# Performance work log

Hardware: AMD Instinct MI355X
Metric: run time of the kernel (lower is better)

The kernel has to match this reference:

```python
import jax, jax.numpy as jnp
from jax import lax
import numpy as np

PAD = 0
V, DW, H, T, B = 30000, 512, 512, 50, 128


def _xavier(key, shape):
    fan_in, fan_out = shape[1], shape[0]
    lim = float(np.sqrt(6.0 / (fan_in + fan_out)))
    return jax.random.uniform(key, shape, jnp.float32, -lim, lim)


def setup_inputs() -> dict:
    key = jax.random.key(0)
    ks = jax.random.split(key, 8)
    return {
        "user": jax.random.randint(ks[0], (B,), 0, 10000),
        "item": jax.random.randint(ks[1], (B,), 0, 10000),
        "review_input": jax.random.randint(ks[2], (T, B), 0, V),
        "review_target": jax.random.randint(ks[3], (T, B), 0, V),
        "word_emb": jax.random.normal(ks[4], (V, DW), jnp.float32) * 0.02,
        "W_ih": _xavier(ks[5], (3 * H, DW)),
        "W_hh": _xavier(ks[6], (3 * H, H)),
        "b_ih": jnp.zeros((3 * H,), jnp.float32),
        "b_hh": jnp.zeros((3 * H,), jnp.float32),
        "W_out": _xavier(ks[7], (V, H)),
        "b_out": jnp.zeros((V,), jnp.float32),
    }


def reference(user, item, review_input, review_target,
              word_emb, W_ih, W_hh, b_ih, b_hh, W_out, b_out):
    n_batch = user.shape[0]
    # embed all timesteps at once: [T, B, DW]
    x = word_emb[review_input]
    # precompute input-to-gate projections: [T, B, 3H]
    xg = jnp.einsum('tbd,gd->tbg', x, W_ih) + b_ih
    h0 = jnp.zeros((n_batch, H), x.dtype)

    def step(h, xg_t):
        hg = h @ W_hh.T + b_hh                      # [B, 3H]
        xr, xz, xn = jnp.split(xg_t, 3, axis=-1)    # PyTorch order: r, z, n
        hr, hz, hn = jnp.split(hg, 3, axis=-1)
        r = jax.nn.sigmoid(xr + hr)
        z = jax.nn.sigmoid(xz + hz)
        n = jnp.tanh(xn + r * hn)
        h_new = (1.0 - z) * n + z * h
        return h_new, h_new

    _, outs = lax.scan(step, h0, xg)                # [T, B, H]
    logits = outs.reshape(-1, H) @ W_out.T + b_out  # [T*B, V]
    tgt = review_target.reshape(-1)
    logp = jax.nn.log_softmax(logits, axis=-1)
    nll = -jnp.take_along_axis(logp, tgt[:, None], axis=1)[:, 0]
    mask = tgt != PAD
    out_loss = jnp.where(mask, nll, 0.0)            # F.cross_entropy reduction='none', ignore_index=PAD
    denom = jnp.maximum(jnp.sum(mask), 1).astype(out_loss.dtype)
    obj = jnp.sum(out_loss) / denom                 # mean over non-ignored tokens
    return out_loss, obj
```

## Files before the change

### kernel.cpp

```cpp
#include <hip/hip_runtime.h>

typedef short short8 __attribute__((ext_vector_type(8)));
typedef float f32x4 __attribute__((ext_vector_type(4)));
typedef float f4 __attribute__((ext_vector_type(4)));
typedef unsigned short ushort_t;

#define VOCAB 30000
#define DW 512
#define KDIM 512
#define HDIM 512
#define G3 1536
#define TT 50
#define BB 128
#define M_ROWS 6400
#define NPAD 30208
#define NT2 472

__device__ __forceinline__ float b2f(ushort_t u){ return __uint_as_float(((unsigned)u)<<16); }
__device__ __forceinline__ ushort_t f2b(float f){
    unsigned u = __float_as_uint(f);
    unsigned r = (u + 0x7fffu + ((u>>16)&1u)) >> 16;
    return (ushort_t)r;
}
__device__ __forceinline__ float sigf(float x){
    float e = __expf(-x);
    return __builtin_amdgcn_rcpf(1.0f + e);
}
__device__ __forceinline__ float tanh_(float x){
    return 2.0f*sigf(2.0f*x) - 1.0f;
}
__device__ __forceinline__ void gload16(const ushort_t* g, char* l){
    __builtin_amdgcn_global_load_lds((const __attribute__((address_space(1))) void*)g,
                                     (__attribute__((address_space(3))) void*)l, 16, 0, 0);
}

__global__ void k_cvt4(const f4* __restrict__ s, ushort_t* __restrict__ d, int n4){
    int i = blockIdx.x*blockDim.x + threadIdx.x;
    if (i < n4){
        f4 v = s[i];
        unsigned lo = (unsigned)f2b(v[0]) | ((unsigned)f2b(v[1]) << 16);
        unsigned hi = (unsigned)f2b(v[2]) | ((unsigned)f2b(v[3]) << 16);
        *(uint2*)(d + (size_t)i*4) = make_uint2(lo, hi);
    }
}
__global__ void k_zero_u(ushort_t* __restrict__ d, int n){
    int i = blockIdx.x*blockDim.x + threadIdx.x;
    if (i < n) d[i] = 0;
}
__global__ void k_gather(const float* __restrict__ emb, const int* __restrict__ idx,
                         ushort_t* __restrict__ x){
    int row = blockIdx.x;
    int v = idx[row];
    const float2* src = (const float2*)(emb + (size_t)v*DW);
    unsigned* dst = (unsigned*)(x + (size_t)row*DW);
    for (int d = threadIdx.x; d < DW/2; d += blockDim.x){
        float2 w = src[d];
        dst[d] = (unsigned)f2b(w.x) | ((unsigned)f2b(w.y) << 16);
    }
}
__global__ void k_biasg(const float* __restrict__ bi, const float* __restrict__ bh,
                        float* __restrict__ bg, float* __restrict__ hf,
                        ushort_t* __restrict__ hb){
    int i = blockIdx.x*blockDim.x + threadIdx.x;
    if (i < G3) bg[i] = bi[i] + (i < 2*HDIM ? bh[i] : 0.0f);
    if (i < BB*HDIM){ hf[i] = 0.0f; hb[i] = 0; }
}

template<int MODE, int NBLK>
__global__ __launch_bounds__(256, 3) void k_gemm5(const ushort_t* __restrict__ A,
        const ushort_t* __restrict__ Bw, const float* __restrict__ bias,
        ushort_t* __restrict__ Cout, float* __restrict__ psum){
    __shared__ ushort_t As[128*32];
    __shared__ ushort_t Bs[128*32];
    const int nwg = NBLK * 50;
    const int q = nwg >> 3;
    int wgid = (blockIdx.x & 7)*q + (blockIdx.x >> 3);
    int band = wgid / (10*NBLK);
    int rr   = wgid % (10*NBLK);
    int nb = rr / 10;
    int mb = band*10 + (rr % 10);
    int n0 = nb*128, m0 = mb*128;

    int lane = threadIdx.x & 63, wv = threadIdx.x >> 6;
    int lo = lane & 15, hi = lane >> 4;
    int wr = wv >> 1, wc = wv & 1;
    f32x4 acc[4][4] = {};
    int xsl = ((lane & 3) ^ ((lane >> 3) & 3)) * 8;
    const ushort_t* gA = A  + (size_t)(m0 + wv*32 + (lane>>2))*KDIM + xsl;
    const ushort_t* gB = Bw + (size_t)(n0 + wv*32 + (lane>>2))*KDIM + xsl;
    char* lA = (char*)As + wv*2048;
    char* lB = (char*)Bs + wv*2048;
    int rchunk = (hi ^ ((lo >> 1) & 3)) * 8;
    for (int kt = 0; kt < 16; ++kt){
        __syncthreads();
        int k0 = kt*32;
        gload16(gA + k0,           lA);
        gload16(gA + 16*KDIM + k0, lA + 1024);
        gload16(gB + k0,           lB);
        gload16(gB + 16*KDIM + k0, lB + 1024);
        __syncthreads();
        short8 av[4], bv[4];
        #pragma unroll
        for (int mi = 0; mi < 4; ++mi)
            av[mi] = *(const short8*)&As[(wr*64 + mi*16 + lo)*32 + rchunk];
        #pragma unroll
        for (int ni = 0; ni < 4; ++ni)
            bv[ni] = *(const short8*)&Bs[(wc*64 + ni*16 + lo)*32 + rchunk];
        #pragma unroll
        for (int mi = 0; mi < 4; ++mi)
            #pragma unroll
            for (int ni = 0; ni < 4; ++ni)
                acc[mi][ni] = __builtin_amdgcn_mfma_f32_16x16x32_bf16(av[mi], bv[ni], acc[mi][ni], 0, 0, 0);
    }

    if (MODE == 0){
        #pragma unroll
        for (int ni = 0; ni < 4; ++ni){
            int n = n0 + wc*64 + ni*16 + lo;
            float bb = bias[n];
            #pragma unroll
            for (int mi = 0; mi < 4; ++mi){
                #pragma unroll
                for (int j = 0; j < 4; ++j){
                    int m = m0 + wr*64 + mi*16 + hi*4 + j;
                    Cout[(size_t)m*G3 + n] = f2b(acc[mi][ni][j] + bb);
                }
            }
        }
    } else {
        const int NT = NBLK*2;
        float bov[4];
        bool valid[4];
        #pragma unroll
        for (int ni = 0; ni < 4; ++ni){
            int col = n0 + wc*64 + ni*16 + lo;
            valid[ni] = (col < VOCAB);
            bov[ni] = valid[ni] ? bias[col] : 0.0f;
        }
        int tile = nb*2 + wc;
        #pragma unroll
        for (int mi = 0; mi < 4; ++mi){
            #pragma unroll
            for (int j = 0; j < 4; ++j){
                float s = 0.0f;
                #pragma unroll
                for (int ni = 0; ni < 4; ++ni)
                    s += valid[ni] ? __expf(acc[mi][ni][j] + bov[ni]) : 0.0f;
                for (int d = 1; d < 16; d <<= 1) s += __shfl_xor(s, d, 64);
                if (lo == 0){
                    int m = m0 + wr*64 + mi*16 + hi*4 + j;
                    psum[(size_t)m*NT + tile] = s;
                }
            }
        }
    }
}

__global__ __launch_bounds__(256) void k_step(const ushort_t* __restrict__ hprev_b,
        const float* __restrict__ hprev_f, const ushort_t* __restrict__ Whh,
        const ushort_t* __restrict__ xg, const float* __restrict__ bh,
        float* __restrict__ hnext_f, ushort_t* __restrict__ hnext_b,
        ushort_t* __restrict__ outs, int t){
    __shared__ float gl[3][4][16][17];
    int tid = threadIdx.x;
    int lane = tid & 63, wv = tid >> 6;
    int lo = lane & 15, hi = lane >> 4;
    int c16 = blockIdx.x * 16;
    int b0  = blockIdx.y * 16;
    f32x4 acc[3] = {};
    const ushort_t* Arow = hprev_b + (size_t)(b0 + lo)*HDIM + wv*128;
    const ushort_t* Bbase = Whh + (size_t)(c16 + lo)*HDIM + wv*128;
    #pragma unroll
    for (int kk = 0; kk < 4; ++kk){
        int k0 = kk*32 + hi*8;
        short8 a = *(const short8*)(Arow + k0);
        #pragma unroll
        for (int g = 0; g < 3; ++g){
            short8 b = *(const short8*)(Bbase + (size_t)g*HDIM*HDIM + k0);
            acc[g] = __builtin_amdgcn_mfma_f32_16x16x32_bf16(a, b, acc[g], 0, 0, 0);
        }
    }
    #pragma unroll
    for (int g = 0; g < 3; ++g)
        #pragma unroll
        for (int j = 0; j < 4; ++j)
            gl[g][wv][hi*4 + j][lo] = acc[g][j];
    __syncthreads();
    int b = tid >> 4, c = tid & 15;
    int bt = b0 + b, cc = c16 + c;
    float hr = gl[0][0][b][c] + gl[0][1][b][c] + gl[0][2][b][c] + gl[0][3][b][c];
    float hz = gl[1][0][b][c] + gl[1][1][b][c] + gl[1][2][b][c] + gl[1][3][b][c];
    float hn = gl[2][0][b][c] + gl[2][1][b][c] + gl[2][2][b][c] + gl[2][3][b][c];
    const ushort_t* xgt = xg + (size_t)t*BB*G3 + (size_t)bt*G3;
    float xr = b2f(xgt[cc]);
    float xz = b2f(xgt[HDIM + cc]);
    float xn = b2f(xgt[2*HDIM + cc]);
    float r  = sigf(hr + xr);
    float z  = sigf(hz + xz);
    float n  = tanh_(xn + r*(hn + bh[2*HDIM + cc]));
    float hold = hprev_f[(size_t)bt*HDIM + cc];
    float hnew = (1.0f - z)*n + z*hold;
    hnext_f[(size_t)bt*HDIM + cc] = hnew;
    ushort_t hv = f2b(hnew);
    hnext_b[(size_t)bt*HDIM + cc] = hv;
    outs[((size_t)t*BB + bt)*HDIM + cc] = hv;
}

__global__ __launch_bounds__(256) void k_loss(const ushort_t* __restrict__ outs,
        const ushort_t* __restrict__ Wo, const float* __restrict__ bo,
        const float* __restrict__ psum, const int* __restrict__ tgt,
        float* __restrict__ out){
    int lane = threadIdx.x & 63, wv = threadIdx.x >> 6;
    int row = blockIdx.x*4 + wv;
    int tg = tgt[row];
    const float* ps = psum + (size_t)row*NT2;
    float S = 0.0f;
    for (int t = lane; t < NT2; t += 64) S += ps[t];
    for (int d = 1; d < 64; d <<= 1) S += __shfl_xor(S, d, 64);
    float lse = __logf(S);
    const ushort_t* a = outs + (size_t)row*HDIM + lane*8;
    const ushort_t* w = Wo + (size_t)tg*DW + lane*8;
    float s = 0.0f;
    #pragma unroll
    for (int j = 0; j < 8; ++j) s += b2f(a[j]) * b2f(w[j]);
    for (int d = 1; d < 64; d <<= 1) s += __shfl_xor(s, d, 64);
    if (lane == 0){
        float logit = s + bo[tg];
        out[row] = (tg != 0) ? (lse - logit) : 0.0f;
    }
}

__global__ __launch_bounds__(1024) void k_obj(const float* __restrict__ loss,
        const int* __restrict__ tgt, float* __restrict__ out){
    __shared__ float ss[1024];
    __shared__ int   sc[1024];
    float s = 0.0f; int c = 0;
    for (int i = threadIdx.x; i < M_ROWS; i += 1024){
        s += loss[i];
        c += (tgt[i] != 0) ? 1 : 0;
    }
    ss[threadIdx.x] = s; sc[threadIdx.x] = c;
    __syncthreads();
    for (int d = 512; d > 0; d >>= 1){
        if (threadIdx.x < (unsigned)d){ ss[threadIdx.x] += ss[threadIdx.x+d]; sc[threadIdx.x] += sc[threadIdx.x+d]; }
        __syncthreads();
    }
    if (threadIdx.x == 0) out[M_ROWS] = ss[0] / (float)(sc[0] > 0 ? sc[0] : 1);
}

extern "C" void kernel_launch(void* const* d_in, const int* in_sizes, int n_in,
                              void* d_out, int out_size, void* d_ws, size_t ws_size,
                              hipStream_t stream) {
    const int*   review_input  = (const int*)d_in[2];
    const int*   review_target = (const int*)d_in[3];
    const float* word_emb = (const float*)d_in[4];
    const float* W_ih = (const float*)d_in[5];
    const float* W_hh = (const float*)d_in[6];
    const float* b_ih = (const float*)d_in[7];
    const float* b_hh = (const float*)d_in[8];
    const float* W_out = (const float*)d_in[9];
    const float* b_out = (const float*)d_in[10];
    float* out = (float*)d_out;
    (void)n_in; (void)in_sizes; (void)out_size; (void)ws_size;

    char* ws = (char*)d_ws;
    size_t off = 0;
    auto alloc = [&](size_t bytes)->char*{
        char* p = ws + off;
        off = (off + bytes + 255) & ~(size_t)255;
        return p;
    };
    ushort_t* Wout_b = (ushort_t*)alloc((size_t)NPAD*DW*2);
    ushort_t* Wih_b  = (ushort_t*)alloc((size_t)G3*DW*2);
    ushort_t* Whh_b  = (ushort_t*)alloc((size_t)G3*HDIM*2);
    ushort_t* outs_b = (ushort_t*)alloc((size_t)M_ROWS*HDIM*2);
    float*    biasg  = (float*)alloc((size_t)G3*4);
    float*    h_f    = (float*)alloc((size_t)2*BB*HDIM*4);
    ushort_t* h_b    = (ushort_t*)alloc((size_t)2*BB*HDIM*2);
    ushort_t* xb     = (ushort_t*)alloc((size_t)M_ROWS*DW*2);
    ushort_t* xg     = (ushort_t*)alloc((size_t)M_ROWS*G3*2);
    float*    psum   = (float*)xb;

    k_cvt4<<<(G3*DW/4+255)/256, 256, 0, stream>>>((const f4*)W_ih, Wih_b, G3*DW/4);
    k_cvt4<<<(G3*HDIM/4+255)/256, 256, 0, stream>>>((const f4*)W_hh, Whh_b, G3*HDIM/4);
    k_cvt4<<<(VOCAB*DW/4+255)/256, 256, 0, stream>>>((const f4*)W_out, Wout_b, VOCAB*DW/4);
    k_zero_u<<<((NPAD-VOCAB)*DW+255)/256, 256, 0, stream>>>(Wout_b + (size_t)VOCAB*DW, (NPAD-VOCAB)*DW);
    k_gather<<<M_ROWS, 256, 0, stream>>>(word_emb, review_input, xb);
    k_biasg<<<(BB*HDIM+255)/256, 256, 0, stream>>>(b_ih, b_hh, biasg, h_f, h_b);

    k_gemm5<0, 12><<<600, 256, 0, stream>>>(xb, Wih_b, biasg, xg, nullptr);

    for (int t = 0; t < TT; ++t){
        int cur = t & 1, nxt = cur ^ 1;
        k_step<<<dim3(HDIM/16, BB/16), 256, 0, stream>>>(h_b + (size_t)cur*BB*HDIM,
                                       h_f + (size_t)cur*BB*HDIM,
                                       Whh_b, xg, b_hh,
                                       h_f + (size_t)nxt*BB*HDIM,
                                       h_b + (size_t)nxt*BB*HDIM,
                                       outs_b, t);
    }

    k_gemm5<1, 236><<<11800, 256, 0, stream>>>(outs_b, Wout_b, b_out, nullptr, psum);
    k_loss<<<M_ROWS/4, 256, 0, stream>>>(outs_b, Wout_b, b_out, psum, review_target, out);
    k_obj<<<1, 1024, 0, stream>>>(out, review_target, out);
}
```

Measured before the change: 513.7 us.

## Overlap output-projection GEMM with GRU recurrence steps in fused per-step kernel

Merges the GRU step kernel and the vocabulary GEMM with partial softmax sums into one kernel launched once per timestep. The first 256 blocks advance the recurrence for step t, while 236 more blocks compute logits and exp-sums for the 128 rows produced at step t-1. This spreads the large output GEMM across the otherwise underused serial recurrence and fills idle CUs. The GEMM tile now uses a 64-wide K slice with XOR swizzle. The cost is larger LDS per block, which can lower occupancy for the step blocks, and mixed work within one launch.

Result: slower. 754.5 us (+46.9%).

```diff
diff --git a/kernel.cpp b/kernel.cpp
--- a/kernel.cpp
+++ b/kernel.cpp
@@ -14,6 +14,7 @@
 #define BB 128
 #define M_ROWS 6400
 #define NPAD 30208
+#define NTILE 236
 #define NT2 472
 
 __device__ __forceinline__ float b2f(ushort_t u){ return __uint_as_float(((unsigned)u)<<16); }
@@ -66,10 +67,10 @@
     if (i < BB*HDIM){ hf[i] = 0.0f; hb[i] = 0; }
 }
 
-template<int MODE, int NBLK>
-__global__ __launch_bounds__(256, 3) void k_gemm5(const ushort_t* __restrict__ A,
+template<int NBLK>
+__global__ __launch_bounds__(256, 3) void k_gemmA(const ushort_t* __restrict__ A,
         const ushort_t* __restrict__ Bw, const float* __restrict__ bias,
-        ushort_t* __restrict__ Cout, float* __restrict__ psum){
+        ushort_t* __restrict__ Cout){
     __shared__ ushort_t As[128*32];
     __shared__ ushort_t Bs[128*32];
     const int nwg = NBLK * 50;
@@ -112,98 +113,148 @@
             for (int ni = 0; ni < 4; ++ni)
                 acc[mi][ni] = __builtin_amdgcn_mfma_f32_16x16x32_bf16(av[mi], bv[ni], acc[mi][ni], 0, 0, 0);
     }
-
-    if (MODE == 0){
-        #pragma unroll
-        for (int ni = 0; ni < 4; ++ni){
-            int n = n0 + wc*64 + ni*16 + lo;
-            float bb = bias[n];
-            #pragma unroll
-            for (int mi = 0; mi < 4; ++mi){
-                #pragma unroll
-                for (int j = 0; j < 4; ++j){
-                    int m = m0 + wr*64 + mi*16 + hi*4 + j;
-                    Cout[(size_t)m*G3 + n] = f2b(acc[mi][ni][j] + bb);
-                }
+    #pragma unroll
+    for (int ni = 0; ni < 4; ++ni){
+        int n = n0 + wc*64 + ni*16 + lo;
+        float bb = bias[n];
+        #pragma unroll
+        for (int mi = 0; mi < 4; ++mi){
+            #pragma unroll
+            for (int j = 0; j < 4; ++j){
+                int m = m0 + wr*64 + mi*16 + hi*4 + j;
+                Cout[(size_t)m*G3 + n] = f2b(acc[mi][ni][j] + bb);
             }
         }
-    } else {
-        const int NT = NBLK*2;
-        float bov[4];
-        bool valid[4];
-        #pragma unroll
-        for (int ni = 0; ni < 4; ++ni){
-            int col = n0 + wc*64 + ni*16 + lo;
-            valid[ni] = (col < VOCAB);
-            bov[ni] = valid[ni] ? bias[col] : 0.0f;
-        }
-        int tile = nb*2 + wc;
-        #pragma unroll
-        for (int mi = 0; mi < 4; ++mi){
-            #pragma unroll
-            for (int j = 0; j < 4; ++j){
-                float s = 0.0f;
-                #pragma unroll
-                for (int ni = 0; ni < 4; ++ni)
-                    s += valid[ni] ? __expf(acc[mi][ni][j] + bov[ni]) : 0.0f;
-                for (int d = 1; d < 16; d <<= 1) s += __shfl_xor(s, d, 64);
-                if (lo == 0){
-                    int m = m0 + wr*64 + mi*16 + hi*4 + j;
-                    psum[(size_t)m*NT + tile] = s;
-                }
-            }
-        }
-    }
-}
-
-__global__ __launch_bounds__(256) void k_step(const ushort_t* __restrict__ hprev_b,
-        const float* __restrict__ hprev_f, const ushort_t* __restrict__ Whh,
-        const ushort_t* __restrict__ xg, const float* __restrict__ bh,
-        float* __restrict__ hnext_f, ushort_t* __restrict__ hnext_b,
-        ushort_t* __restrict__ outs, int t){
+    }
+}
+
+__global__ __launch_bounds__(256) void k_fused(
+        const ushort_t* __restrict__ hprev_b, const float* __restrict__ hprev_f,
+        const ushort_t* __restrict__ Whh, const ushort_t* __restrict__ xg,
+        const float* __restrict__ bh, float* __restrict__ hnext_f,
+        ushort_t* __restrict__ hnext_b, ushort_t* __restrict__ outs,
+        const ushort_t* __restrict__ Wo, const float* __restrict__ bo,
+        float* __restrict__ psum, int t){
+    __shared__ ushort_t As[128*64];
+    __shared__ ushort_t Bs[128*64];
     __shared__ float gl[3][4][16][17];
     int tid = threadIdx.x;
     int lane = tid & 63, wv = tid >> 6;
     int lo = lane & 15, hi = lane >> 4;
-    int c16 = blockIdx.x * 16;
-    int b0  = blockIdx.y * 16;
-    f32x4 acc[3] = {};
-    const ushort_t* Arow = hprev_b + (size_t)(b0 + lo)*HDIM + wv*128;
-    const ushort_t* Bbase = Whh + (size_t)(c16 + lo)*HDIM + wv*128;
+
+    if (blockIdx.x < 256){
+        if (t >= TT) return;
+        int c16 = (blockIdx.x & 31) * 16;
+        int b0  = (blockIdx.x >> 5) * 16;
+        f32x4 acc[3] = {};
+        const ushort_t* Arow = hprev_b + (size_t)(b0 + lo)*HDIM + wv*128;
+        const ushort_t* Bbase = Whh + (size_t)(c16 + lo)*HDIM + wv*128;
+        #pragma unroll
+        for (int kk = 0; kk < 4; ++kk){
+            int k0 = kk*32 + hi*8;
+            short8 a = *(const short8*)(Arow + k0);
+            #pragma unroll
+            for (int g = 0; g < 3; ++g){
+                short8 b = *(const short8*)(Bbase + (size_t)g*HDIM*HDIM + k0);
+                acc[g] = __builtin_amdgcn_mfma_f32_16x16x32_bf16(a, b, acc[g], 0, 0, 0);
+            }
+        }
+        #pragma unroll
+        for (int g = 0; g < 3; ++g)
+            #pragma unroll
+            for (int j = 0; j < 4; ++j)
+                gl[g][wv][hi*4 + j][lo] = acc[g][j];
+        __syncthreads();
+        int b = tid >> 4, c = tid & 15;
+        int bt = b0 + b, cc = c16 + c;
+        float hr = gl[0][0][b][c] + gl[0][1][b][c] + gl[0][2][b][c] + gl[0][3][b][c];
+        float hz = gl[1][0][b][c] + gl[1][1][b][c] + gl[1][2][b][c] + gl[1][3][b][c];
+        float hn = gl[2][0][b][c] + gl[2][1][b][c] + gl[2][2][b][c] + gl[2][3][b][c];
+        const ushort_t* xgt = xg + (size_t)t*BB*G3 + (size_t)bt*G3;
+        float xr = b2f(xgt[cc]);
+        float xz = b2f(xgt[HDIM + cc]);
+        float xn = b2f(xgt[2*HDIM + cc]);
+        float r  = sigf(hr + xr);
+        float z  = sigf(hz + xz);
+        float n  = tanh_(xn + r*(hn + bh[2*HDIM + cc]));
+        float hold = hprev_f[(size_t)bt*HDIM + cc];
+        float hnew = (1.0f - z)*n + z*hold;
+        hnext_f[(size_t)bt*HDIM + cc] = hnew;
+        ushort_t hv = f2b(hnew);
+        hnext_b[(size_t)bt*HDIM + cc] = hv;
+        outs[((size_t)t*BB + bt)*HDIM + cc] = hv;
+        return;
+    }
+
+    if (t == 0) return;
+    int nb = blockIdx.x - 256;
+    int tm = t - 1;
+    int m0 = tm * 128;
+    int n0 = nb * 128;
+    int wr = wv >> 1, wc = wv & 1;
+    f32x4 acc[4][4] = {};
+    int srow = lane >> 3;
+    int xslot = (lane & 7) ^ srow;
+    const ushort_t* gA = outs + (size_t)(m0 + wv*32 + srow)*KDIM + xslot*8;
+    const ushort_t* gB = Wo   + (size_t)(n0 + wv*32 + srow)*KDIM + xslot*8;
+    char* lA = (char*)As + (size_t)(wv*32)*128;
+    char* lB = (char*)Bs + (size_t)(wv*32)*128;
+    for (int kt = 0; kt < 8; ++kt){
+        __syncthreads();
+        int k0 = kt*64;
+        #pragma unroll
+        for (int cc4 = 0; cc4 < 4; ++cc4){
+            gload16(gA + (size_t)cc4*8*KDIM + k0, lA + cc4*8*128);
+            gload16(gB + (size_t)cc4*8*KDIM + k0, lB + cc4*8*128);
+        }
+        __syncthreads();
+        short8 av[4][2], bv[4][2];
+        #pragma unroll
+        for (int mi = 0; mi < 4; ++mi){
+            int rrow = wr*64 + mi*16 + lo;
+            #pragma unroll
+            for (int ks = 0; ks < 2; ++ks)
+                av[mi][ks] = *(const short8*)&As[rrow*64 + (((ks*4+hi) ^ (lo&7)))*8];
+        }
+        #pragma unroll
+        for (int ni = 0; ni < 4; ++ni){
+            int rrow = wc*64 + ni*16 + lo;
+            #pragma unroll
+            for (int ks = 0; ks < 2; ++ks)
+                bv[ni][ks] = *(const short8*)&Bs[rrow*64 + (((ks*4+hi) ^ (lo&7)))*8];
+        }
+        #pragma unroll
+        for (int mi = 0; mi < 4; ++mi)
+            #pragma unroll
+            for (int ni = 0; ni < 4; ++ni){
+                acc[mi][ni] = __builtin_amdgcn_mfma_f32_16x16x32_bf16(av[mi][0], bv[ni][0], acc[mi][ni], 0, 0, 0);
+                acc[mi][ni] = __builtin_amdgcn_mfma_f32_16x16x32_bf16(av[mi][1], bv[ni][1], acc[mi][ni], 0, 0, 0);
+            }
+    }
+    float bov[4];
+    bool valid[4];
     #pragma unroll
-    for (int kk = 0; kk < 4; ++kk){
-        int k0 = kk*32 + hi*8;
-        short8 a = *(const short8*)(Arow + k0);
-        #pragma unroll
-        for (int g = 0; g < 3; ++g){
-            short8 b = *(const short8*)(Bbase + (size_t)g*HDIM*HDIM + k0);
-            acc[g] = __builtin_amdgcn_mfma_f32_16x16x32_bf16(a, b, acc[g], 0, 0, 0);
-        }
-    }
+    for (int ni = 0; ni < 4; ++ni){
+        int col = n0 + wc*64 + ni*16 + lo;
+        valid[ni] = (col < VOCAB);
+        bov[ni] = valid[ni] ? bo[col] : 0.0f;
+    }
+    int tile = nb*2 + wc;
     #pragma unroll
-    for (int g = 0; g < 3; ++g)
-        #pragma unroll
-        for (int j = 0; j < 4; ++j)
-            gl[g][wv][hi*4 + j][lo] = acc[g][j];
-    __syncthreads();
-    int b = tid >> 4, c = tid & 15;
-    int bt = b0 + b, cc = c16 + c;
-    float hr = gl[0][0][b][c] + gl[0][1][b][c] + gl[0][2][b][c] + gl[0][3][b][c];
-    float hz = gl[1][0][b][c] + gl[1][1][b][c] + gl[1][2][b][c] + gl[1][3][b][c];
-    float hn = gl[2][0][b][c] + gl[2][1][b][c] + gl[2][2][b][c] + gl[2][3][b][c];
-    const ushort_t* xgt = xg + (size_t)t*BB*G3 + (size_t)bt*G3;
-    float xr = b2f(xgt[cc]);
-    float xz = b2f(xgt[HDIM + cc]);
-    float xn = b2f(xgt[2*HDIM + cc]);
-    float r  = sigf(hr + xr);
-    float z  = sigf(hz + xz);
-    float n  = tanh_(xn + r*(hn + bh[2*HDIM + cc]));
-    float hold = hprev_f[(size_t)bt*HDIM + cc];
-    float hnew = (1.0f - z)*n + z*hold;
-    hnext_f[(size_t)bt*HDIM + cc] = hnew;
-    ushort_t hv = f2b(hnew);
-    hnext_b[(size_t)bt*HDIM + cc] = hv;
-    outs[((size_t)t*BB + bt)*HDIM + cc] = hv;
+    for (int mi = 0; mi < 4; ++mi){
+        #pragma unroll
+        for (int j = 0; j < 4; ++j){
+            float s = 0.0f;
+            #pragma unroll
+            for (int ni = 0; ni < 4; ++ni)
+                s += valid[ni] ? __expf(acc[mi][ni][j] + bov[ni]) : 0.0f;
+            for (int d = 1; d < 16; d <<= 1) s += __shfl_xor(s, d, 64);
+            if (lo == 0){
+                int m = m0 + wr*64 + mi*16 + hi*4 + j;
+                psum[(size_t)m*NT2 + tile] = s;
+            }
+        }
+    }
 }
 
 __global__ __launch_bounds__(256) void k_loss(const ushort_t* __restrict__ outs,
@@ -288,19 +339,17 @@
     k_gather<<<M_ROWS, 256, 0, stream>>>(word_emb, review_input, xb);
     k_biasg<<<(BB*HDIM+255)/256, 256, 0, stream>>>(b_ih, b_hh, biasg, h_f, h_b);
 
-    k_gemm5<0, 12><<<600, 256, 0, stream>>>(xb, Wih_b, biasg, xg, nullptr);
-
-    for (int t = 0; t < TT; ++t){
+    k_gemmA<12><<<600, 256, 0, stream>>>(xb, Wih_b, biasg, xg);
+
+    for (int t = 0; t <= TT; ++t){
         int cur = t & 1, nxt = cur ^ 1;
-        k_step<<<dim3(HDIM/16, BB/16), 256, 0, stream>>>(h_b + (size_t)cur*BB*HDIM,
-                                       h_f + (size_t)cur*BB*HDIM,
-                                       Whh_b, xg, b_hh,
-                                       h_f + (size_t)nxt*BB*HDIM,
-                                       h_b + (size_t)nxt*BB*HDIM,
-                                       outs_b, t);
-    }
-
-    k_gemm5<1, 236><<<11800, 256, 0, stream>>>(outs_b, Wout_b, b_out, nullptr, psum);
+        k_fused<<<256 + NTILE, 256, 0, stream>>>(
+            h_b + (size_t)cur*BB*HDIM, h_f + (size_t)cur*BB*HDIM,
+            Whh_b, xg, b_hh,
+            h_f + (size_t)nxt*BB*HDIM, h_b + (size_t)nxt*BB*HDIM,
+            outs_b, Wout_b, b_out, psum, t);
+    }
+
     k_loss<<<M_ROWS/4, 256, 0, stream>>>(outs_b, Wout_b, b_out, psum, review_target, out);
     k_obj<<<1, 1024, 0, stream>>>(out, review_target, out);
 }
```
